# Kernel optimization log

Measured on AMD Instinct MI355X. Metric: run time of the kernel, lower is better.

Reference implementation:

```python
import jax, jax.numpy as jnp
import numpy as np

N_NODES = 50000
N_EDGES = 800000
IN_CH = 64
HID = 64
EDGE_DIM = 16


def _glorot(key, shape):
    fan_in, fan_out = shape[0], shape[1]
    lim = (6.0 / (fan_in + fan_out)) ** 0.5
    return jax.random.uniform(key, shape, jnp.float32, -lim, lim)


def setup_inputs() -> dict:
    key = jax.random.key(0)
    ks = jax.random.split(key, 12)
    x = jax.random.normal(ks[0], (N_NODES, IN_CH), jnp.float32)
    edge_index = jax.random.randint(ks[1], (2, N_EDGES), 0, N_NODES, jnp.int64)
    edge_attr = jax.random.normal(ks[2], (N_EDGES, EDGE_DIM), jnp.float32)
    # SAGEConv1: lin_l (aggregated neighbors, with bias) + lin_r (root, no bias)
    W1l = _glorot(ks[3], (IN_CH, HID)); b1l = jnp.zeros((HID,), jnp.float32)
    W1r = _glorot(ks[4], (IN_CH, HID))
    # SAGEConv2
    W2l = _glorot(ks[5], (HID, HID)); b2l = jnp.zeros((HID,), jnp.float32)
    W2r = _glorot(ks[6], (HID, HID))
    # edge MLP: Linear(2*HID+EDGE_DIM -> HID), ReLU, Linear(HID -> 1)
    Wm1 = _glorot(ks[7], (2 * HID + EDGE_DIM, HID))
    bm1 = jnp.zeros((HID,), jnp.float32)
    Wm2 = _glorot(ks[8], (HID, 1))
    bm2 = jnp.zeros((1,), jnp.float32)
    return dict(x=x, edge_index=edge_index, edge_attr=edge_attr,
                W1l=W1l, b1l=b1l, W1r=W1r,
                W2l=W2l, b2l=b2l, W2r=W2r,
                Wm1=Wm1, bm1=bm1, Wm2=Wm2, bm2=bm2)


def _sage_conv(x, src, dst, deg_inv, Wl, bl, Wr):
    # mean aggregation of source-node features at destination nodes
    n = x.shape[0]
    agg = jax.ops.segment_sum(x[src], dst, num_segments=n)  # [N, d]
    agg = agg * deg_inv  # mean over incoming edges
    return agg @ Wl + bl + x @ Wr


def reference(x, edge_index, edge_attr, W1l, b1l, W1r, W2l, b2l, W2r, Wm1, bm1, Wm2, bm2):
    src, dst = edge_index[0], edge_index[1]
    n = x.shape[0]
    # in-degree (over dst), clamped to 1 as in PyG mean aggregation
    deg = jax.ops.segment_sum(jnp.ones((src.shape[0],), x.dtype), dst, num_segments=n)
    deg_inv = (1.0 / jnp.maximum(deg, 1.0))[:, None]  # [N,1]

    h = jax.nn.relu(_sage_conv(x, src, dst, deg_inv, W1l, b1l, W1r))
    h = jax.nn.relu(_sage_conv(h, src, dst, deg_inv, W2l, b2l, W2r))

    # gather endpoint embeddings + concat with edge features -> MLP score
    edge_input = jnp.concatenate([h[src], h[dst], edge_attr], axis=-1)  # [E, 2H+De]
    hidden = jax.nn.relu(edge_input @ Wm1 + bm1)
    return (hidden @ Wm2 + bm2).squeeze(-1)  # [E]
```

## Files before the change

### kernel.cpp

```cpp
#include <hip/hip_runtime.h>
#include <hip/hip_bf16.h>


#define C 64
#define KP 168
#define SK 136
#define TILE_E 64
#define WSHIFT 12

typedef short short8 __attribute__((ext_vector_type(8)));
typedef float f32x4 __attribute__((ext_vector_type(4)));

__device__ __forceinline__ unsigned short f2bf(float f) {
    unsigned int u = __float_as_uint(f);
    return (unsigned short)((u + 0x7FFFu + ((u >> 16) & 1u)) >> 16);
}
__device__ __forceinline__ unsigned int pack2(float lo, float hi) {
    return (unsigned int)f2bf(lo) | ((unsigned int)f2bf(hi) << 16);
}
__device__ __forceinline__ float bflo(unsigned int u) { return __uint_as_float(u << 16); }
__device__ __forceinline__ float bfhi(unsigned int u) { return __uint_as_float(u & 0xFFFF0000u); }

__global__ void prep(const int* __restrict__ dst, int* __restrict__ degi,
                     const float* __restrict__ ea, unsigned short* __restrict__ eaB,
                     const float* __restrict__ x, unsigned short* __restrict__ xB,
                     int E, int nx8, int doEa) {
    int i = blockIdx.x * blockDim.x + threadIdx.x;
    if (i < E) atomicAdd(&degi[dst[i]], 1);
    if (doEa && i < 2 * E) {
        const float4* p = (const float4*)(ea + (size_t)i * 8);
        float4 a = p[0], b = p[1];
        uint4 o;
        o.x = pack2(a.x, a.y); o.y = pack2(a.z, a.w);
        o.z = pack2(b.x, b.y); o.w = pack2(b.z, b.w);
        *(uint4*)(eaB + (size_t)i * 8) = o;
    }
    if (i < nx8) {
        const float4* p = (const float4*)(x + (size_t)i * 8);
        float4 a = p[0], b = p[1];
        uint4 o;
        o.x = pack2(a.x, a.y); o.y = pack2(a.z, a.w);
        o.z = pack2(b.x, b.y); o.w = pack2(b.z, b.w);
        *(uint4*)(xB + (size_t)i * 8) = o;
    }
}

__global__ __launch_bounds__(256) void scan_partial(const int* __restrict__ degi,
        int* __restrict__ rowptr, int* __restrict__ partials, int N) {
    __shared__ int sWs[4];
    int t = threadIdx.x, b = blockIdx.x;
    int g0 = b * 1024 + t * 4;
    int v0 = (g0 + 0 < N) ? degi[g0 + 0] : 0;
    int v1 = (g0 + 1 < N) ? degi[g0 + 1] : 0;
    int v2 = (g0 + 2 < N) ? degi[g0 + 2] : 0;
    int v3 = (g0 + 3 < N) ? degi[g0 + 3] : 0;
    int tsum = v0 + v1 + v2 + v3;
    int lane = t & 63, w = t >> 6;
    int incl = tsum;
    #pragma unroll
    for (int m = 1; m < 64; m <<= 1) {
        int y = __shfl_up(incl, m, 64);
        if (lane >= m) incl += y;
    }
    if (lane == 63) sWs[w] = incl;
    __syncthreads();
    int wprefix = 0;
    for (int i = 0; i < w; ++i) wprefix += sWs[i];
    int run = wprefix + incl - tsum;
    if (g0 + 0 < N) rowptr[g0 + 0] = run; run += v0;
    if (g0 + 1 < N) rowptr[g0 + 1] = run; run += v1;
    if (g0 + 2 < N) rowptr[g0 + 2] = run; run += v2;
    if (g0 + 3 < N) rowptr[g0 + 3] = run;
    if (t == 255) partials[b] = wprefix + incl;
}

__global__ __launch_bounds__(256) void scan_add_fused(int* __restrict__ rowptr,
        const int* __restrict__ partials, int* __restrict__ cursor,
        const int* __restrict__ degi, float* __restrict__ deg_inv,
        int N, int E, int nb) {
    __shared__ int sOff[64];
    int t = threadIdx.x;
    if (t < 64) {
        int v = (t < nb) ? partials[t] : 0;
        int incl = v;
        #pragma unroll
        for (int m = 1; m < 64; m <<= 1) {
            int y = __shfl_up(incl, m, 64);
            if (t >= m) incl += y;
        }
        sOff[t] = incl - v;
    }
    __syncthreads();
    int i = blockIdx.x * 256 + t;
    if (i < N) {
        int r = rowptr[i] + sOff[i >> 10];
        rowptr[i] = r;
        cursor[i] = r;
        deg_inv[i] = 1.0f / fmaxf((float)degi[i], 1.0f);
    }
    if (i == 0) rowptr[N] = E;
}

__global__ __launch_bounds__(256) void fill_csr_xcd(const int* __restrict__ src,
        const int* __restrict__ dst, int* __restrict__ cursor,
        int* __restrict__ eSrc, int E) {
    int g = blockIdx.x & 7;
    int tid = (blockIdx.x >> 3) * 256 + threadIdx.x;
    int stride = (gridDim.x >> 3) * 256;
    for (int e = tid; e < E; e += stride) {
        int d = dst[e];
        if (((d >> WSHIFT) & 7) == g) {
            int pos = atomicAdd(&cursor[d], 1);
            eSrc[pos] = src[e];
        }
    }
}

__global__ __launch_bounds__(256) void csr_agg_bf16(const unsigned short* __restrict__ fB,
        const int* __restrict__ rowptr, const int* __restrict__ eSrc,
        const float* __restrict__ deg_inv, unsigned short* __restrict__ aggB, int N) {
    int node = blockIdx.x * 4 + (threadIdx.x >> 6);
    if (node >= N) return;
    int lane = threadIdx.x & 63;
    int s8 = lane >> 3, ci = lane & 7;
    int row = rowptr[node], end = rowptr[node + 1];
    float a[8] = {0.f, 0.f, 0.f, 0.f, 0.f, 0.f, 0.f, 0.f};
    int j = row;
    for (; j + 16 <= end; j += 16) {
        int sA = eSrc[j + s8];
        int sB = eSrc[j + 8 + s8];
        uint4 vA = *(const uint4*)(fB + (size_t)sA * C + ci * 8);
        uint4 vB = *(const uint4*)(fB + (size_t)sB * C + ci * 8);
        a[0] += bflo(vA.x); a[1] += bfhi(vA.x);
        a[2] += bflo(vA.y); a[3] += bfhi(vA.y);
        a[4] += bflo(vA.z); a[5] += bfhi(vA.z);
        a[6] += bflo(vA.w); a[7] += bfhi(vA.w);
        a[0] += bflo(vB.x); a[1] += bfhi(vB.x);
        a[2] += bflo(vB.y); a[3] += bfhi(vB.y);
        a[4] += bflo(vB.z); a[5] += bfhi(vB.z);
        a[6] += bflo(vB.w); a[7] += bfhi(vB.w);
    }
    for (; j < end; j += 8) {
        if (j + s8 < end) {
            int s = eSrc[j + s8];
            uint4 v = *(const uint4*)(fB + (size_t)s * C + ci * 8);
            a[0] += bflo(v.x); a[1] += bfhi(v.x);
            a[2] += bflo(v.y); a[3] += bfhi(v.y);
            a[4] += bflo(v.z); a[5] += bfhi(v.z);
            a[6] += bflo(v.w); a[7] += bfhi(v.w);
        }
    }
    #pragma unroll
    for (int m = 8; m < 64; m <<= 1)
        #pragma unroll
        for (int k = 0; k < 8; ++k)
            a[k] += __shfl_xor(a[k], m, 64);
    if (s8 == 0) {
        float di = deg_inv[node];
        uint4 o;
        o.x = pack2(a[0] * di, a[1] * di);
        o.y = pack2(a[2] * di, a[3] * di);
        o.z = pack2(a[4] * di, a[5] * di);
        o.w = pack2(a[6] * di, a[7] * di);
        *(uint4*)(aggB + (size_t)node * C + ci * 8) = o;
    }
}

__global__ __launch_bounds__(256) void dense_mfma(
        const unsigned short* __restrict__ aB, const unsigned short* __restrict__ xB,
        const float* __restrict__ Wl, const float* __restrict__ Wr,
        const float* __restrict__ bl, unsigned short* __restrict__ hOut, int N) {
    __shared__ unsigned short sW[C * SK];
    __shared__ unsigned short sAB[C * SK];
    int t = threadIdx.x;
    int lane = t & 63, w = t >> 6;
    int l15 = lane & 15, quad = lane >> 4;
    int n0 = blockIdx.x * 64;

    for (int i = t; i < 128 * C; i += 256) {
        int k = i >> 6, n = i & 63;
        float v = (k < C) ? Wl[k * C + n] : Wr[(k - C) * C + n];
        sW[n * SK + k] = f2bf(v);
    }
    for (int i = t; i < 64 * 16; i += 256) {
        int r = i >> 4, ch = i & 15;
        int node = n0 + r;
        uint4 v = {0u, 0u, 0u, 0u};
        if (node < N)
            v = (ch < 8) ? *(const uint4*)(aB + (size_t)node * C + ch * 8)
                         : *(const uint4*)(xB + (size_t)node * C + (ch - 8) * 8);
        *(uint4*)&sAB[r * SK + ch * 8] = v;
    }
    __syncthreads();

    short8 bW[4][4];
    #pragma unroll
    for (int t4 = 0; t4 < 4; ++t4)
        #pragma unroll
        for (int kc = 0; kc < 4; ++kc)
            bW[t4][kc] = *(const short8*)&sW[(t4 * 16 + l15) * SK + kc * 32 + quad * 8];
    float blr[4];
    #pragma unroll
    for (int t4 = 0; t4 < 4; ++t4) blr[t4] = bl[t4 * 16 + l15];

    f32x4 acc[4] = {{0.f, 0.f, 0.f, 0.f}, {0.f, 0.f, 0.f, 0.f},
                    {0.f, 0.f, 0.f, 0.f}, {0.f, 0.f, 0.f, 0.f}};
    #pragma unroll
    for (int kc = 0; kc < 4; ++kc) {
        short8 a = *(const short8*)&sAB[(w * 16 + l15) * SK + kc * 32 + quad * 8];
        #pragma unroll
        for (int t4 = 0; t4 < 4; ++t4)
            acc[t4] = __builtin_amdgcn_mfma_f32_16x16x32_bf16(a, bW[t4][kc], acc[t4], 0, 0, 0);
    }
    __syncthreads();

    #pragma unroll
    for (int t4 = 0; t4 < 4; ++t4)
        #pragma unroll
        for (int r = 0; r < 4; ++r) {
            int rl = w * 16 + quad * 4 + r;
            sW[rl * 72 + t4 * 16 + l15] = f2bf(fmaxf(acc[t4][r] + blr[t4], 0.f));
        }
    __syncthreads();
    for (int i = t; i < 64 * 8; i += 256) {
        int r = i >> 3, c8 = i & 7;
        int node = n0 + r;
        if (node < N)
            *(uint4*)(hOut + (size_t)node * C + c8 * 8) = *(const uint4*)&sW[r * 72 + c8 * 8];
    }
}

template <bool EAB>
__device__ __forceinline__ void gather_rows(const unsigned short* __restrict__ hB,
        const unsigned short* __restrict__ eaB, const float* __restrict__ ea,
        int s, int d, int idxc, int quad,
        uint4& u0, uint4& u1, uint4& u2, uint4& u3, uint4& u4) {
    const uint4* ps = (const uint4*)(hB + (size_t)s * C);
    const uint4* pd = (const uint4*)(hB + (size_t)d * C);
    u0 = ps[quad];
    u1 = ps[4 + quad];
    u2 = pd[quad];
    u3 = pd[4 + quad];
    u4.x = 0u; u4.y = 0u; u4.z = 0u; u4.w = 0u;
    if (quad < 2) {
        if (EAB) {
            u4 = *(const uint4*)(eaB + (size_t)idxc * 16 + quad * 8);
        } else {
            const float4* pe = (const float4*)(ea + (size_t)idxc * 16 + quad * 8);
            float4 f0 = pe[0], f1 = pe[1];
            u4.x = pack2(f0.x, f0.y); u4.y = pack2(f0.z, f0.w);
            u4.z = pack2(f1.x, f1.y); u4.w = pack2(f1.z, f1.w);
        }
    }
}

template <bool EAB>
__global__ __launch_bounds__(256) void edge_mlp_pipe(
        const unsigned short* __restrict__ hB, const int* __restrict__ src,
        const int* __restrict__ dst, const float* __restrict__ ea,
        const unsigned short* __restrict__ eaB,
        const float* __restrict__ Wm1, const float* __restrict__ bm1,
        const float* __restrict__ Wm2, const float* __restrict__ bm2,
        float* __restrict__ out, int E, int nTiles) {
    __shared__ unsigned short sW[C * KP];
    int t = threadIdx.x;
    int lane = t & 63, w = t >> 6;
    int l15 = lane & 15, quad = lane >> 4;

    for (int i = t; i < C * 3; i += 256) {
        int r = i / 3, cc = 144 + (i % 3) * 8;
        uint4 z = {0u, 0u, 0u, 0u};
        *(uint4*)&sW[r * KP + cc] = z;
    }
    for (int i = t; i < 144 * C; i += 256) {
        int k = i >> 6, n = i & 63;
        sW[n * KP + k] = f2bf(Wm1[i]);
    }
    __syncthreads();

    short8 aW[4][5];
    #pragma unroll
    for (int t4 = 0; t4 < 4; ++t4)
        #pragma unroll
        for (int kc = 0; kc < 5; ++kc)
            aW[t4][kc] = *(const short8*)&sW[(t4 * 16 + l15) * KP + kc * 32 + quad * 8];
    float4 bmv[4], w2v[4];
    #pragma unroll
    for (int t4 = 0; t4 < 4; ++t4) {
        bmv[t4] = *(const float4*)&bm1[t4 * 16 + quad * 4];
        w2v[t4] = *(const float4*)&Wm2[t4 * 16 + quad * 4];
    }
    float bb = bm2[0];

    int stride = gridDim.x;
    int lbase = w * 16 + l15;

    int tile = blockIdx.x;
    int idxc = min(tile * TILE_E + lbase, E - 1);
    int s = src[idxc], d = dst[idxc];
    int tileN = tile + stride;
    int idxNc = (tileN < nTiles) ? min(tileN * TILE_E + lbase, E - 1) : idxc;
    int sN = src[idxNc], dN = dst[idxNc];
    uint4 cu0, cu1, cu2, cu3, cu4;
    gather_rows<EAB>(hB, eaB, ea, s, d, idxc, quad, cu0, cu1, cu2, cu3, cu4);

    while (true) {
        bool hasNext = (tileN < nTiles);
        uint4 nu0, nu1, nu2, nu3, nu4;
        gather_rows<EAB>(hB, eaB, ea, sN, dN, idxNc, quad, nu0, nu1, nu2, nu3, nu4);
        int tileNN = tileN + stride;
        int idxNNc = (tileNN < nTiles) ? min(tileNN * TILE_E + lbase, E - 1) : idxNc;
        int sNN = src[idxNNc], dNN = dst[idxNNc];

        short8 b0 = *(short8*)&cu0, b1 = *(short8*)&cu1, b2 = *(short8*)&cu2,
               b3 = *(short8*)&cu3, b4 = *(short8*)&cu4;
        f32x4 acc[4] = {{0.f, 0.f, 0.f, 0.f}, {0.f, 0.f, 0.f, 0.f},
                        {0.f, 0.f, 0.f, 0.f}, {0.f, 0.f, 0.f, 0.f}};
        #pragma unroll
        for (int t4 = 0; t4 < 4; ++t4) {
            acc[t4] = __builtin_amdgcn_mfma_f32_16x16x32_bf16(aW[t4][0], b0, acc[t4], 0, 0, 0);
            acc[t4] = __builtin_amdgcn_mfma_f32_16x16x32_bf16(aW[t4][1], b1, acc[t4], 0, 0, 0);
            acc[t4] = __builtin_amdgcn_mfma_f32_16x16x32_bf16(aW[t4][2], b2, acc[t4], 0, 0, 0);
            acc[t4] = __builtin_amdgcn_mfma_f32_16x16x32_bf16(aW[t4][3], b3, acc[t4], 0, 0, 0);
            acc[t4] = __builtin_amdgcn_mfma_f32_16x16x32_bf16(aW[t4][4], b4, acc[t4], 0, 0, 0);
        }

        float v = 0.f;
        #pragma unroll
        for (int t4 = 0; t4 < 4; ++t4) {
            v += fmaxf(acc[t4][0] + bmv[t4].x, 0.f) * w2v[t4].x;
            v += fmaxf(acc[t4][1] + bmv[t4].y, 0.f) * w2v[t4].y;
            v += fmaxf(acc[t4][2] + bmv[t4].z, 0.f) * w2v[t4].z;
            v += fmaxf(acc[t4][3] + bmv[t4].w, 0.f) * w2v[t4].w;
        }
        v += __shfl_xor(v, 16, 64);
        v += __shfl_xor(v, 32, 64);
        int e = tile * TILE_E + w * 16 + l15;
        if (quad == 0 && e < E) out[e] = v + bb;

        if (!hasNext) break;
        tile = tileN; tileN = tileNN;
        idxc = idxNc; idxNc = idxNNc;
        s = sN; sN = sNN; d = dN; dN = dNN;
        cu0 = nu0; cu1 = nu1; cu2 = nu2; cu3 = nu3; cu4 = nu4;
    }
}

extern "C" void kernel_launch(void* const* d_in, const int* in_sizes, int n_in,
                              void* d_out, int out_size, void* d_ws, size_t ws_size,
                              hipStream_t stream) {
    const float* x   = (const float*)d_in[0];
    const int*   ei  = (const int*)d_in[1];
    const float* ea  = (const float*)d_in[2];
    const float* W1l = (const float*)d_in[3];
    const float* b1l = (const float*)d_in[4];
    const float* W1r = (const float*)d_in[5];
    const float* W2l = (const float*)d_in[6];
    const float* b2l = (const float*)d_in[7];
    const float* W2r = (const float*)d_in[8];
    const float* Wm1 = (const float*)d_in[9];
    const float* bm1 = (const float*)d_in[10];
    const float* Wm2 = (const float*)d_in[11];
    const float* bm2 = (const float*)d_in[12];
    float* out = (float*)d_out;

    const int N = in_sizes[0] / C;
    const int E = in_sizes[1] / 2;
    const int* src = ei;
    const int* dst = ei + E;

    char* wsb = (char*)d_ws;
    int npad = (N + 1023) & ~1023;
    float* deg_inv = (float*)wsb;                wsb += (size_t)npad * 4;
    unsigned short* xB   = (unsigned short*)wsb; wsb += (size_t)npad * C * 2;
    unsigned short* h1B  = (unsigned short*)wsb; wsb += (size_t)npad * C * 2;
    unsigned short* h2B  = (unsigned short*)wsb; wsb += (size_t)npad * C * 2;
    unsigned short* aggB = (unsigned short*)wsb; wsb += (size_t)npad * C * 2;
    int* degi    = (int*)wsb;                    wsb += (size_t)npad * 4;
    int* rowptr  = (int*)wsb;                    wsb += (size_t)(npad + 64) * 4;
    int* cursor  = (int*)wsb;                    wsb += (size_t)npad * 4;
    int* eSrc    = (int*)wsb;                    wsb += (size_t)E * 4;
    int* partials = (int*)wsb;                   wsb += 64 * 4;
    unsigned short* eaB = (unsigned short*)wsb;
    size_t used = (size_t)(wsb - (char*)d_ws);
    int useEaB = (ws_size >= used + (size_t)E * 16 * 2) ? 1 : 0;

    int tpb = 256;
    int nb = (N + 1023) / 1024;
    int nx8 = N * C / 8;

    hipMemsetAsync(degi, 0, (size_t)N * sizeof(int), stream);
    int prepN = (2 * E > nx8) ? 2 * E : nx8;
    prep<<<(prepN + tpb - 1) / tpb, tpb, 0, stream>>>(dst, degi, ea, eaB, x, xB, E, nx8, useEaB);
    scan_partial<<<nb, tpb, 0, stream>>>(degi, rowptr, partials, N);
    scan_add_fused<<<(N + tpb - 1) / tpb, tpb, 0, stream>>>(rowptr, partials, cursor,
            degi, deg_inv, N, E, nb);
    fill_csr_xcd<<<1024, tpb, 0, stream>>>(src, dst, cursor, eSrc, E);

    csr_agg_bf16<<<(N + 3) / 4, tpb, 0, stream>>>(xB, rowptr, eSrc, deg_inv, aggB, N);
    dense_mfma<<<(N + 63) / 64, tpb, 0, stream>>>(aggB, xB, W1l, W1r, b1l, h1B, N);

    csr_agg_bf16<<<(N + 3) / 4, tpb, 0, stream>>>(h1B, rowptr, eSrc, deg_inv, aggB, N);
    dense_mfma<<<(N + 63) / 64, tpb, 0, stream>>>(aggB, h1B, W2l, W2r, b2l, h2B, N);

    int nTiles = (E + TILE_E - 1) / TILE_E;
    int grid = nTiles < 2048 ? nTiles : 2048;
    if (useEaB)
        edge_mlp_pipe<true><<<grid, tpb, 0, stream>>>(h2B, src, dst, ea, eaB,
                Wm1, bm1, Wm2, bm2, out, E, nTiles);
    else
        edge_mlp_pipe<false><<<grid, tpb, 0, stream>>>(h2B, src, dst, ea, eaB,
                Wm1, bm1, Wm2, bm2, out, E, nTiles);
}
```

Measured before the change: 304.5 us.

## Read edge-MLP weights from LDS per tile to cut registers and raise occupancy

The edge MLP kernel no longer keeps the 20 short8 weight fragments, the bias and the second-layer weights in registers. It re-reads them from shared memory on every tile, which frees about 80+ VGPRs. A launch-bounds hint of 7 blocks per CU is added, and the grid is resized to 1792 (7 per CU on 256 CUs) so more waves can hide gather latency. The cost is extra LDS traffic per MFMA and LDS capacity that may limit residency.

```diff
diff --git a/kernel.cpp b/kernel.cpp
--- a/kernel.cpp
+++ b/kernel.cpp
@@ -255,7 +255,7 @@
 }
 
 template <bool EAB>
-__global__ __launch_bounds__(256) void edge_mlp_pipe(
+__global__ __launch_bounds__(256, 7) void edge_mlp_pipe(
         const unsigned short* __restrict__ hB, const int* __restrict__ src,
         const int* __restrict__ dst, const float* __restrict__ ea,
         const unsigned short* __restrict__ eaB,
@@ -263,6 +263,7 @@
         const float* __restrict__ Wm2, const float* __restrict__ bm2,
         float* __restrict__ out, int E, int nTiles) {
     __shared__ unsigned short sW[C * KP];
+    __shared__ float sBm[C], sW2[C];
     int t = threadIdx.x;
     int lane = t & 63, w = t >> 6;
     int l15 = lane & 15, quad = lane >> 4;
@@ -276,22 +277,10 @@
         int k = i >> 6, n = i & 63;
         sW[n * KP + k] = f2bf(Wm1[i]);
     }
-    __syncthreads();
-
-    short8 aW[4][5];
-    #pragma unroll
-    for (int t4 = 0; t4 < 4; ++t4)
-        #pragma unroll
-        for (int kc = 0; kc < 5; ++kc)
-            aW[t4][kc] = *(const short8*)&sW[(t4 * 16 + l15) * KP + kc * 32 + quad * 8];
-    float4 bmv[4], w2v[4];
-    #pragma unroll
-    for (int t4 = 0; t4 < 4; ++t4) {
-        bmv[t4] = *(const float4*)&bm1[t4 * 16 + quad * 4];
-        w2v[t4] = *(const float4*)&Wm2[t4 * 16 + quad * 4];
-    }
+    if (t < C) { sBm[t] = bm1[t]; sW2[t] = Wm2[t]; }
+    __syncthreads();
+
     float bb = bm2[0];
-
     int stride = gridDim.x;
     int lbase = w * 16 + l15;
 
@@ -318,20 +307,28 @@
                         {0.f, 0.f, 0.f, 0.f}, {0.f, 0.f, 0.f, 0.f}};
         #pragma unroll
         for (int t4 = 0; t4 < 4; ++t4) {
-            acc[t4] = __builtin_amdgcn_mfma_f32_16x16x32_bf16(aW[t4][0], b0, acc[t4], 0, 0, 0);
-            acc[t4] = __builtin_amdgcn_mfma_f32_16x16x32_bf16(aW[t4][1], b1, acc[t4], 0, 0, 0);
-            acc[t4] = __builtin_amdgcn_mfma_f32_16x16x32_bf16(aW[t4][2], b2, acc[t4], 0, 0, 0);
-            acc[t4] = __builtin_amdgcn_mfma_f32_16x16x32_bf16(aW[t4][3], b3, acc[t4], 0, 0, 0);
-            acc[t4] = __builtin_amdgcn_mfma_f32_16x16x32_bf16(aW[t4][4], b4, acc[t4], 0, 0, 0);
+            const unsigned short* wrow = &sW[(t4 * 16 + l15) * KP + quad * 8];
+            acc[t4] = __builtin_amdgcn_mfma_f32_16x16x32_bf16(
+                    *(const short8*)(wrow), b0, acc[t4], 0, 0, 0);
+            acc[t4] = __builtin_amdgcn_mfma_f32_16x16x32_bf16(
+                    *(const short8*)(wrow + 32), b1, acc[t4], 0, 0, 0);
+            acc[t4] = __builtin_amdgcn_mfma_f32_16x16x32_bf16(
+                    *(const short8*)(wrow + 64), b2, acc[t4], 0, 0, 0);
+            acc[t4] = __builtin_amdgcn_mfma_f32_16x16x32_bf16(
+                    *(const short8*)(wrow + 96), b3, acc[t4], 0, 0, 0);
+            acc[t4] = __builtin_amdgcn_mfma_f32_16x16x32_bf16(
+                    *(const short8*)(wrow + 128), b4, acc[t4], 0, 0, 0);
         }
 
         float v = 0.f;
         #pragma unroll
         for (int t4 = 0; t4 < 4; ++t4) {
-            v += fmaxf(acc[t4][0] + bmv[t4].x, 0.f) * w2v[t4].x;
-            v += fmaxf(acc[t4][1] + bmv[t4].y, 0.f) * w2v[t4].y;
-            v += fmaxf(acc[t4][2] + bmv[t4].z, 0.f) * w2v[t4].z;
-            v += fmaxf(acc[t4][3] + bmv[t4].w, 0.f) * w2v[t4].w;
+            float4 bm4 = *(const float4*)&sBm[t4 * 16 + quad * 4];
+            float4 w24 = *(const float4*)&sW2[t4 * 16 + quad * 4];
+            v += fmaxf(acc[t4][0] + bm4.x, 0.f) * w24.x;
+            v += fmaxf(acc[t4][1] + bm4.y, 0.f) * w24.y;
+            v += fmaxf(acc[t4][2] + bm4.z, 0.f) * w24.z;
+            v += fmaxf(acc[t4][3] + bm4.w, 0.f) * w24.w;
         }
         v += __shfl_xor(v, 16, 64);
         v += __shfl_xor(v, 32, 64);
@@ -404,7 +401,7 @@
     dense_mfma<<<(N + 63) / 64, tpb, 0, stream>>>(aggB, h1B, W2l, W2r, b2l, h2B, N);
 
     int nTiles = (E + TILE_E - 1) / TILE_E;
-    int grid = nTiles < 2048 ? nTiles : 2048;
+    int grid = nTiles < 1792 ? nTiles : 1792;
     if (useEaB)
         edge_mlp_pipe<true><<<grid, tpb, 0, stream>>>(h2B, src, dst, ea, eaB,
                 Wm1, bm1, Wm2, bm2, out, E, nTiles);
```

New measurement: 521.2 us. 71.2% more time.
